# Optimization experiments

Hardware: AMD Instinct MI355X
Metric: run time of the kernel (lower is better)

Reference implementation:

```python
import jax, jax.numpy as jnp
import numpy as np

N_NODES = 50000
N_FEAT = 256
HIDDEN = 256
N_EDGES = 800000


def gcn_conv(x, edge_index, W, b):
    """PyG GCNConv: out = D^-1/2 (A+I) D^-1/2 (x @ W) + b."""
    n = x.shape[0]
    loop = jnp.arange(n, dtype=edge_index.dtype)
    src = jnp.concatenate([edge_index[0], loop])  # [E+N]
    dst = jnp.concatenate([edge_index[1], loop])  # [E+N]
    deg = jax.ops.segment_sum(jnp.ones_like(dst, dtype=x.dtype), dst, num_segments=n)
    dinv = jnp.where(deg > 0, jax.lax.rsqrt(deg), 0.0)
    norm = dinv[src] * dinv[dst]                  # [E+N]
    h = x @ W                                     # [N, out]
    msg = h[src] * norm[:, None]                  # gather + scale
    out = jax.ops.segment_sum(msg, dst, num_segments=n)  # scatter-add
    return out + b


def setup_inputs() -> dict:
    key = jax.random.key(0)
    ks = jax.random.split(key, 8)
    x = jax.random.normal(ks[0], (N_NODES, N_FEAT), dtype=jnp.float32)
    train_pos_edge_index = jax.random.randint(ks[1], (2, N_EDGES), 0, N_NODES, dtype=jnp.int64)
    pos_edge_index = jax.random.randint(ks[2], (2, N_EDGES), 0, N_NODES, dtype=jnp.int64)
    neg_edge_index = jax.random.randint(ks[3], (2, N_EDGES), 0, N_NODES, dtype=jnp.int64)
    # Glorot-style init for GCN weights
    W1 = jax.random.normal(ks[4], (N_FEAT, HIDDEN), dtype=jnp.float32) * (1.0 / np.sqrt(N_FEAT))
    b1 = jnp.zeros((HIDDEN,), dtype=jnp.float32)
    W2 = jax.random.normal(ks[5], (HIDDEN, HIDDEN // 2), dtype=jnp.float32) * (1.0 / np.sqrt(HIDDEN))
    b2 = jnp.zeros((HIDDEN // 2,), dtype=jnp.float32)
    return {"x": x, "train_pos_edge_index": train_pos_edge_index,
            "pos_edge_index": pos_edge_index, "neg_edge_index": neg_edge_index,
            "W1": W1, "b1": b1, "W2": W2, "b2": b2}


def reference(x, train_pos_edge_index, pos_edge_index, neg_edge_index, W1, b1, W2, b2):
    # encode
    h = jax.nn.relu(gcn_conv(x, train_pos_edge_index, W1, b1))
    z = gcn_conv(h, train_pos_edge_index, W2, b2)  # [N, HIDDEN//2]
    # decode: dot product over concatenated pos+neg edges
    edge_index = jnp.concatenate([pos_edge_index, neg_edge_index], axis=-1)  # [2, 2E]
    logits = jnp.sum(z[edge_index[0]] * z[edge_index[1]], axis=-1)           # [2E]
    return logits
```

## Files before the change

### kernel.cpp

```cpp
#include <hip/hip_runtime.h>
#include <hip/hip_fp16.h>


#define NFEAT 256
#define HID   256
#define OUTF  128
#define SCAN_T 1024

typedef _Float16 f16x8 __attribute__((ext_vector_type(8)));
typedef float    f32x4 __attribute__((ext_vector_type(4)));

__global__ void k_init_deg(float* __restrict__ deg, int n) {
    int i = blockIdx.x * blockDim.x + threadIdx.x;
    if (i < n) deg[i] = 1.0f;
}

__global__ void k_count_deg(const int* __restrict__ ei, float* __restrict__ deg, int E) {
    int e = blockIdx.x * blockDim.x + threadIdx.x;
    if (e < E) atomicAdd(&deg[ei[E + e]], 1.0f);
}

__global__ __launch_bounds__(SCAN_T) void k_scan(
        float* __restrict__ deg_dinv, int* __restrict__ rowptr,
        int* __restrict__ cursor, int n) {
    __shared__ int swsum[16];
    __shared__ int s_total;
    __shared__ int s_chunk;
    const int t    = threadIdx.x;
    const int wave = t >> 6;
    const int lane = t & 63;
    if (t == 0) s_total = 0;

    for (int base = 0; base < n; base += SCAN_T) {
        int i = base + t;
        float dg = 1.0f;
        int v = 0;
        if (i < n) { dg = deg_dinv[i]; v = (int)dg - 1; }
        int sc = v;
#pragma unroll
        for (int off = 1; off < 64; off <<= 1) {
            int y = __shfl_up(sc, off);
            if (lane >= off) sc += y;
        }
        if (lane == 63) swsum[wave] = sc;
        __syncthreads();
        if (t < 16) {
            int w = swsum[t];
            int scw = w;
#pragma unroll
            for (int off = 1; off < 16; off <<= 1) {
                int y = __shfl_up(scw, off);
                if (t >= off) scw += y;
            }
            swsum[t] = scw - w;
            if (t == 15) s_chunk = scw;
        }
        __syncthreads();
        int rp = s_total + swsum[wave] + (sc - v);
        if (i < n) {
            rowptr[i] = rp;
            cursor[i] = rp;
            deg_dinv[i] = rsqrtf(dg);
        }
        __syncthreads();
        if (t == 0) s_total += s_chunk;
        __syncthreads();
    }
    if (t == 0) rowptr[n] = s_total;
}

__global__ void k_fill(const int* __restrict__ ei, int* __restrict__ cursor,
                       int* __restrict__ eidx, int E) {
    int e = blockIdx.x * blockDim.x + threadIdx.x;
    if (e < E) {
        int s = ei[e];
        int d = ei[E + e];
        int p = atomicAdd(&cursor[d], 1);
        eidx[p] = s;
    }
}

__global__ __launch_bounds__(256) void k_wt(const float* __restrict__ W,
                                            __half* __restrict__ Wt, int K, int M) {
    __shared__ float tile[32][33];
    int k0 = blockIdx.x * 32, m0 = blockIdx.y * 32;
    int tx = threadIdx.x & 31, ty = threadIdx.x >> 5;
#pragma unroll
    for (int r = 0; r < 4; ++r)
        tile[ty + r * 8][tx] = W[(size_t)(k0 + ty + r * 8) * M + m0 + tx];
    __syncthreads();
#pragma unroll
    for (int r = 0; r < 4; ++r)
        Wt[(size_t)(m0 + ty + r * 8) * K + k0 + tx] = __float2half(tile[tx][ty + r * 8]);
}

template <int MT, bool AF32>
__global__ __launch_bounds__(256) void k_gemm_mfma(
        const void* __restrict__ Aptr, const __half* __restrict__ Wt,
        const float* __restrict__ dinv, __half* __restrict__ outp,
        int n, int K, int M) {
    constexpr int BM = 2 * MT * 16;
    __shared__ __half As[BM][40];
    __shared__ __half Bs[128][40];
    __shared__ __half Cs[4][16][72];

    const int t    = threadIdx.x;
    const int wave = t >> 6;
    const int lane = t & 63;
    const int row0 = blockIdx.x * BM;
    const int col0 = blockIdx.y * 128;
    const int wm = wave >> 1, wn = wave & 1;
    const int lr = lane & 15;
    const int kq = lane >> 4;

    f32x4 acc[MT][4];
#pragma unroll
    for (int i = 0; i < MT; ++i)
#pragma unroll
        for (int j = 0; j < 4; ++j) acc[i][j] = (f32x4){0.f, 0.f, 0.f, 0.f};

    for (int k0 = 0; k0 < K; k0 += 32) {
        if (AF32) {
            const float* A = (const float*)Aptr;
#pragma unroll
            for (int it = 0; it < BM * 8 / 256; ++it) {
                int q = t + it * 256;
                int r = q >> 3, c4 = q & 7;
                int gr = min(row0 + r, n - 1);
                float4 v = *(const float4*)&A[(size_t)gr * K + k0 + c4 * 4];
                __half2* dst = (__half2*)&As[r][c4 * 4];
                dst[0] = __floats2half2_rn(v.x, v.y);
                dst[1] = __floats2half2_rn(v.z, v.w);
            }
        } else {
            const __half* A = (const __half*)Aptr;
#pragma unroll
            for (int it = 0; it < BM * 4 / 256; ++it) {
                int q = t + it * 256;
                int r = q >> 2, c8 = q & 3;
                int gr = min(row0 + r, n - 1);
                *(float4*)&As[r][c8 * 8] = *(const float4*)&A[(size_t)gr * K + k0 + c8 * 8];
            }
        }
#pragma unroll
        for (int it = 0; it < 2; ++it) {
            int q = t + it * 256;
            int r = q >> 2, c8 = q & 3;
            *(float4*)&Bs[r][c8 * 8] = *(const float4*)&Wt[(size_t)(col0 + r) * K + k0 + c8 * 8];
        }
        __syncthreads();

        f16x8 b[4];
#pragma unroll
        for (int j = 0; j < 4; ++j)
            b[j] = *(const f16x8*)&Bs[wn * 64 + j * 16 + lr][kq * 8];
#pragma unroll
        for (int i = 0; i < MT; ++i) {
            f16x8 a = *(const f16x8*)&As[wm * MT * 16 + i * 16 + lr][kq * 8];
#pragma unroll
            for (int j = 0; j < 4; ++j)
                acc[i][j] = __builtin_amdgcn_mfma_f32_16x16x32_f16(a, b[j], acc[i][j], 0, 0, 0);
        }
        __syncthreads();
    }

#pragma unroll
    for (int i = 0; i < MT; ++i) {
        int gr0 = row0 + wm * MT * 16 + i * 16;
        float dv[4];
#pragma unroll
        for (int r = 0; r < 4; ++r)
            dv[r] = dinv[min(gr0 + kq * 4 + r, n - 1)];
        __syncthreads();
#pragma unroll
        for (int j = 0; j < 4; ++j)
#pragma unroll
            for (int r = 0; r < 4; ++r)
                Cs[wave][kq * 4 + r][j * 16 + lr] = __float2half(acc[i][j][r] * dv[r]);
        __syncthreads();
        int r1 = lane >> 3, c1 = (lane & 7) * 8;
#pragma unroll
        for (int h = 0; h < 2; ++h) {
            int grow = gr0 + r1 + h * 8;
            if (grow < n)
                *(float4*)&outp[(size_t)grow * M + col0 + wn * 64 + c1] =
                    *(const float4*)&Cs[wave][r1 + h * 8][c1];
        }
    }
}

__global__ void k_agg1(const int* __restrict__ rowptr, const int* __restrict__ eidx,
                       const __half* __restrict__ g, const float* __restrict__ dinv,
                       const float* __restrict__ bias, __half* __restrict__ out, int n) {
    int wid  = (int)(((size_t)blockIdx.x * blockDim.x + threadIdx.x) >> 6);
    int lane = threadIdx.x & 63;
    if (wid >= n) return;
    int j   = rowptr[wid];
    int end = rowptr[wid + 1];
    float sc = dinv[wid];

    union HF2 { float2 f; __half2 h[2]; };
    float4 acc;
    {
        HF2 u; u.f = ((const float2*)(g + (size_t)wid * HID))[lane];
        float2 lo = __half22float2(u.h[0]);
        float2 hi = __half22float2(u.h[1]);
        acc = make_float4(lo.x, lo.y, hi.x, hi.y);
    }
    for (; j + 1 < end; j += 2) {
        int s0 = eidx[j];
        int s1 = eidx[j + 1];
        HF2 u0; u0.f = ((const float2*)(g + (size_t)s0 * HID))[lane];
        HF2 u1; u1.f = ((const float2*)(g + (size_t)s1 * HID))[lane];
        float2 a0 = __half22float2(u0.h[0]), a1 = __half22float2(u0.h[1]);
        float2 c0 = __half22float2(u1.h[0]), c1 = __half22float2(u1.h[1]);
        acc.x += a0.x + c0.x; acc.y += a0.y + c0.y;
        acc.z += a1.x + c1.x; acc.w += a1.y + c1.y;
    }
    if (j < end) {
        int s0 = eidx[j];
        HF2 u0; u0.f = ((const float2*)(g + (size_t)s0 * HID))[lane];
        float2 a0 = __half22float2(u0.h[0]), a1 = __half22float2(u0.h[1]);
        acc.x += a0.x; acc.y += a0.y; acc.z += a1.x; acc.w += a1.y;
    }
    float4 b = ((const float4*)bias)[lane];
    HF2 r;
    r.h[0] = __floats2half2_rn(fmaxf(sc * acc.x + b.x, 0.f), fmaxf(sc * acc.y + b.y, 0.f));
    r.h[1] = __floats2half2_rn(fmaxf(sc * acc.z + b.z, 0.f), fmaxf(sc * acc.w + b.w, 0.f));
    ((float2*)(out + (size_t)wid * HID))[lane] = r.f;
}

__global__ void k_agg2(const int* __restrict__ rowptr, const int* __restrict__ eidx,
                       const __half* __restrict__ g, const float* __restrict__ dinv,
                       const float* __restrict__ bias, __half* __restrict__ out, int n) {
    int wid  = (int)(((size_t)blockIdx.x * blockDim.x + threadIdx.x) >> 6);
    int lane = threadIdx.x & 63;
    if (wid >= n) return;
    int j   = rowptr[wid];
    int end = rowptr[wid + 1];
    float sc = dinv[wid];

    float2 acc = __half22float2(((const __half2*)(g + (size_t)wid * OUTF))[lane]);
    for (; j + 1 < end; j += 2) {
        int s0 = eidx[j];
        int s1 = eidx[j + 1];
        float2 v0 = __half22float2(((const __half2*)(g + (size_t)s0 * OUTF))[lane]);
        float2 v1 = __half22float2(((const __half2*)(g + (size_t)s1 * OUTF))[lane]);
        acc.x += v0.x + v1.x; acc.y += v0.y + v1.y;
    }
    if (j < end) {
        int s0 = eidx[j];
        float2 v0 = __half22float2(((const __half2*)(g + (size_t)s0 * OUTF))[lane]);
        acc.x += v0.x; acc.y += v0.y;
    }
    float2 b = ((const float2*)bias)[lane];
    __half2 r = __floats2half2_rn(sc * acc.x + b.x, sc * acc.y + b.y);
    ((__half2*)(out + (size_t)wid * OUTF))[lane] = r;
}

__global__ void k_decode(const int* __restrict__ pos, const int* __restrict__ neg,
                         const __half* __restrict__ z, float* __restrict__ out, int E) {
    size_t gid = (size_t)blockIdx.x * blockDim.x + threadIdx.x;
    int e  = (int)(gid >> 4);
    int sl = (int)(threadIdx.x & 15);
    if (e >= 2 * E) return;
    int a, b;
    if (e < E) { a = pos[e];     b = pos[E + e]; }
    else       { a = neg[e - E]; b = neg[e];     }
    union HF4 { float4 f; __half2 h[4]; };
    HF4 ua, ub;
    ua.f = ((const float4*)(z + (size_t)a * OUTF))[sl];
    ub.f = ((const float4*)(z + (size_t)b * OUTF))[sl];
    float p = 0.f;
#pragma unroll
    for (int k = 0; k < 4; ++k) {
        float2 fa = __half22float2(ua.h[k]);
        float2 fb = __half22float2(ub.h[k]);
        p += fa.x * fb.x + fa.y * fb.y;
    }
    p += __shfl_xor(p, 1);
    p += __shfl_xor(p, 2);
    p += __shfl_xor(p, 4);
    p += __shfl_xor(p, 8);
    if (sl == 0) out[e] = p;
}

extern "C" void kernel_launch(void* const* d_in, const int* in_sizes, int n_in,
                              void* d_out, int out_size, void* d_ws, size_t ws_size,
                              hipStream_t stream) {
    const float* x   = (const float*)d_in[0];
    const int*   tei = (const int*)d_in[1];
    const int*   pos = (const int*)d_in[2];
    const int*   neg = (const int*)d_in[3];
    const float* W1  = (const float*)d_in[4];
    const float* b1  = (const float*)d_in[5];
    const float* W2  = (const float*)d_in[6];
    const float* b2  = (const float*)d_in[7];
    float* out = (float*)d_out;

    const int N = in_sizes[0] / NFEAT;
    const int E = in_sizes[1] / 2;

    char* ws = (char*)d_ws;
    size_t off = 0;
    __half* g1h = (__half*)(ws + off);
    __half* g2h = (__half*)(ws + off);
    __half* zh  = (__half*)(ws + off + (size_t)N * OUTF * 2);
    off += (size_t)N * HID * 2;
    __half* h1h = (__half*)(ws + off);  off += (size_t)N * HID * 2;
    float*  dinv = (float*)(ws + off);  off += (size_t)N * 4;
    int* rowptr = (int*)(ws + off);     off += (size_t)(N + 1) * 4;
    int* cursor = (int*)(ws + off);     off += (size_t)N * 4;
    int* eidx   = (int*)(ws + off);     off += (size_t)E * 4;
    __half* W1t = (__half*)(ws + off);  off += (size_t)NFEAT * HID * 2;
    __half* W2t = (__half*)(ws + off);  off += (size_t)HID * OUTF * 2;

    { dim3 g(NFEAT / 32, HID / 32);  k_wt<<<g, 256, 0, stream>>>(W1, W1t, NFEAT, HID); }
    { dim3 g(HID / 32, OUTF / 32);   k_wt<<<g, 256, 0, stream>>>(W2, W2t, HID, OUTF); }

    k_init_deg<<<(N + 255) / 256, 256, 0, stream>>>(dinv, N);
    k_count_deg<<<(E + 255) / 256, 256, 0, stream>>>(tei, dinv, E);
    k_scan<<<1, SCAN_T, 0, stream>>>(dinv, rowptr, cursor, N);
    k_fill<<<(E + 255) / 256, 256, 0, stream>>>(tei, cursor, eidx, E);

    {
        dim3 grid((N + 127) / 128, HID / 128);
        k_gemm_mfma<4, true><<<grid, 256, 0, stream>>>(x, W1t, dinv, g1h, N, NFEAT, HID);
        size_t nth = (size_t)N * 64;
        k_agg1<<<(int)((nth + 255) / 256), 256, 0, stream>>>(
            rowptr, eidx, g1h, dinv, b1, h1h, N);
    }

    {
        dim3 grid((N + 63) / 64, OUTF / 128);
        k_gemm_mfma<2, false><<<grid, 256, 0, stream>>>(h1h, W2t, dinv, g2h, N, HID, OUTF);
        size_t nth = (size_t)N * 64;
        k_agg2<<<(int)((nth + 255) / 256), 256, 0, stream>>>(
            rowptr, eidx, g2h, dinv, b2, zh, N);
    }

    {
        size_t nth = (size_t)2 * E * 16;
        k_decode<<<(int)((nth + 255) / 256), 256, 0, stream>>>(pos, neg, zh, out, E);
    }
}
```

Measured before the change: 495.6 us.

## Store GEMM outputs in feature-sliced layout and aggregate per slice

The GEMM epilogue now writes its output in a column-sliced layout: 8 slices of 32 (layer 1) or 16 (layer 2) features, each slice stored contiguously across all nodes. The aggregation kernels are rewritten so consecutive blocks handle one slice for a group of nodes. Each neighbour gather then touches a 64- or 32-byte segment inside a smaller per-slice working set, which is meant to improve cache hit rates for the random gathers. The cost is more gather instructions per edge, each fetching fewer bytes, and edge indices are reread once per slice.

```diff
diff --git a/kernel.cpp b/kernel.cpp
--- a/kernel.cpp
+++ b/kernel.cpp
@@ -94,7 +94,7 @@
         Wt[(size_t)(m0 + ty + r * 8) * K + k0 + tx] = __float2half(tile[tx][ty + r * 8]);
 }
 
-template <int MT, bool AF32>
+template <int MT, bool AF32, int SWL>
 __global__ __launch_bounds__(256) void k_gemm_mfma(
         const void* __restrict__ Aptr, const __half* __restrict__ Wt,
         const float* __restrict__ dinv, __half* __restrict__ outp,
@@ -164,6 +164,7 @@
         __syncthreads();
     }
 
+    constexpr int SW = 1 << SWL;
 #pragma unroll
     for (int i = 0; i < MT; ++i) {
         int gr0 = row0 + wm * MT * 16 + i * 16;
@@ -182,80 +183,76 @@
 #pragma unroll
         for (int h = 0; h < 2; ++h) {
             int grow = gr0 + r1 + h * 8;
-            if (grow < n)
-                *(float4*)&outp[(size_t)grow * M + col0 + wn * 64 + c1] =
-                    *(const float4*)&Cs[wave][r1 + h * 8][c1];
+            if (grow < n) {
+                int col = col0 + wn * 64 + c1;
+                size_t oidx = ((size_t)(col >> SWL) * n + grow) * SW + (col & (SW - 1));
+                *(float4*)&outp[oidx] = *(const float4*)&Cs[wave][r1 + h * 8][c1];
+            }
         }
     }
 }
 
 __global__ void k_agg1(const int* __restrict__ rowptr, const int* __restrict__ eidx,
-                       const __half* __restrict__ g, const float* __restrict__ dinv,
+                       const __half* __restrict__ g1s, const float* __restrict__ dinv,
                        const float* __restrict__ bias, __half* __restrict__ out, int n) {
-    int wid  = (int)(((size_t)blockIdx.x * blockDim.x + threadIdx.x) >> 6);
-    int lane = threadIdx.x & 63;
-    if (wid >= n) return;
-    int j   = rowptr[wid];
-    int end = rowptr[wid + 1];
-    float sc = dinv[wid];
-
-    union HF2 { float2 f; __half2 h[2]; };
-    float4 acc;
-    {
-        HF2 u; u.f = ((const float2*)(g + (size_t)wid * HID))[lane];
-        float2 lo = __half22float2(u.h[0]);
-        float2 hi = __half22float2(u.h[1]);
-        acc = make_float4(lo.x, lo.y, hi.x, hi.y);
-    }
+    const int slice = blockIdx.x & 7;
+    const int node  = (blockIdx.x >> 3) * 16 + (threadIdx.x >> 4);
+    const int sl    = threadIdx.x & 15;
+    if (node >= n) return;
+    int j   = rowptr[node];
+    int end = rowptr[node + 1];
+    float sc = dinv[node];
+    const __half* base = g1s + (size_t)slice * n * 32 + sl * 2;
+
+    float2 acc = __half22float2(*(const __half2*)&base[(size_t)node * 32]);
     for (; j + 1 < end; j += 2) {
         int s0 = eidx[j];
         int s1 = eidx[j + 1];
-        HF2 u0; u0.f = ((const float2*)(g + (size_t)s0 * HID))[lane];
-        HF2 u1; u1.f = ((const float2*)(g + (size_t)s1 * HID))[lane];
-        float2 a0 = __half22float2(u0.h[0]), a1 = __half22float2(u0.h[1]);
-        float2 c0 = __half22float2(u1.h[0]), c1 = __half22float2(u1.h[1]);
-        acc.x += a0.x + c0.x; acc.y += a0.y + c0.y;
-        acc.z += a1.x + c1.x; acc.w += a1.y + c1.y;
+        float2 v0 = __half22float2(*(const __half2*)&base[(size_t)s0 * 32]);
+        float2 v1 = __half22float2(*(const __half2*)&base[(size_t)s1 * 32]);
+        acc.x += v0.x + v1.x; acc.y += v0.y + v1.y;
     }
     if (j < end) {
         int s0 = eidx[j];
-        HF2 u0; u0.f = ((const float2*)(g + (size_t)s0 * HID))[lane];
-        float2 a0 = __half22float2(u0.h[0]), a1 = __half22float2(u0.h[1]);
-        acc.x += a0.x; acc.y += a0.y; acc.z += a1.x; acc.w += a1.y;
-    }
-    float4 b = ((const float4*)bias)[lane];
-    HF2 r;
-    r.h[0] = __floats2half2_rn(fmaxf(sc * acc.x + b.x, 0.f), fmaxf(sc * acc.y + b.y, 0.f));
-    r.h[1] = __floats2half2_rn(fmaxf(sc * acc.z + b.z, 0.f), fmaxf(sc * acc.w + b.w, 0.f));
-    ((float2*)(out + (size_t)wid * HID))[lane] = r.f;
+        float2 v0 = __half22float2(*(const __half2*)&base[(size_t)s0 * 32]);
+        acc.x += v0.x; acc.y += v0.y;
+    }
+    int f = slice * 32 + sl * 2;
+    float2 b = *(const float2*)&bias[f];
+    __half2 r = __floats2half2_rn(fmaxf(sc * acc.x + b.x, 0.f),
+                                  fmaxf(sc * acc.y + b.y, 0.f));
+    *(__half2*)&out[(size_t)node * HID + f] = r;
 }
 
 __global__ void k_agg2(const int* __restrict__ rowptr, const int* __restrict__ eidx,
-                       const __half* __restrict__ g, const float* __restrict__ dinv,
+                       const __half* __restrict__ g2s, const float* __restrict__ dinv,
                        const float* __restrict__ bias, __half* __restrict__ out, int n) {
-    int wid  = (int)(((size_t)blockIdx.x * blockDim.x + threadIdx.x) >> 6);
-    int lane = threadIdx.x & 63;
-    if (wid >= n) return;
-    int j   = rowptr[wid];
-    int end = rowptr[wid + 1];
-    float sc = dinv[wid];
-
-    float2 acc = __half22float2(((const __half2*)(g + (size_t)wid * OUTF))[lane]);
+    const int slice = blockIdx.x & 7;
+    const int node  = (blockIdx.x >> 3) * 32 + (threadIdx.x >> 3);
+    const int sl    = threadIdx.x & 7;
+    if (node >= n) return;
+    int j   = rowptr[node];
+    int end = rowptr[node + 1];
+    float sc = dinv[node];
+    const __half* base = g2s + (size_t)slice * n * 16 + sl * 2;
+
+    float2 acc = __half22float2(*(const __half2*)&base[(size_t)node * 16]);
     for (; j + 1 < end; j += 2) {
         int s0 = eidx[j];
         int s1 = eidx[j + 1];
-        float2 v0 = __half22float2(((const __half2*)(g + (size_t)s0 * OUTF))[lane]);
-        float2 v1 = __half22float2(((const __half2*)(g + (size_t)s1 * OUTF))[lane]);
+        float2 v0 = __half22float2(*(const __half2*)&base[(size_t)s0 * 16]);
+        float2 v1 = __half22float2(*(const __half2*)&base[(size_t)s1 * 16]);
         acc.x += v0.x + v1.x; acc.y += v0.y + v1.y;
     }
     if (j < end) {
         int s0 = eidx[j];
-        float2 v0 = __half22float2(((const __half2*)(g + (size_t)s0 * OUTF))[lane]);
+        float2 v0 = __half22float2(*(const __half2*)&base[(size_t)s0 * 16]);
         acc.x += v0.x; acc.y += v0.y;
     }
-    float2 b = ((const float2*)bias)[lane];
+    int f = slice * 16 + sl * 2;
+    float2 b = *(const float2*)&bias[f];
     __half2 r = __floats2half2_rn(sc * acc.x + b.x, sc * acc.y + b.y);
-    ((__half2*)(out + (size_t)wid * OUTF))[lane] = r;
+    *(__half2*)&out[(size_t)node * OUTF + f] = r;
 }
 
 __global__ void k_decode(const int* __restrict__ pos, const int* __restrict__ neg,
@@ -303,8 +300,8 @@
 
     char* ws = (char*)d_ws;
     size_t off = 0;
-    __half* g1h = (__half*)(ws + off);
-    __half* g2h = (__half*)(ws + off);
+    __half* g1s = (__half*)(ws + off);
+    __half* g2s = (__half*)(ws + off);
     __half* zh  = (__half*)(ws + off + (size_t)N * OUTF * 2);
     off += (size_t)N * HID * 2;
     __half* h1h = (__half*)(ws + off);  off += (size_t)N * HID * 2;
@@ -325,18 +322,16 @@
 
     {
         dim3 grid((N + 127) / 128, HID / 128);
-        k_gemm_mfma<4, true><<<grid, 256, 0, stream>>>(x, W1t, dinv, g1h, N, NFEAT, HID);
-        size_t nth = (size_t)N * 64;
-        k_agg1<<<(int)((nth + 255) / 256), 256, 0, stream>>>(
-            rowptr, eidx, g1h, dinv, b1, h1h, N);
+        k_gemm_mfma<4, true, 5><<<grid, 256, 0, stream>>>(x, W1t, dinv, g1s, N, NFEAT, HID);
+        int nblk = 8 * ((N + 15) / 16);
+        k_agg1<<<nblk, 256, 0, stream>>>(rowptr, eidx, g1s, dinv, b1, h1h, N);
     }
 
     {
         dim3 grid((N + 63) / 64, OUTF / 128);
-        k_gemm_mfma<2, false><<<grid, 256, 0, stream>>>(h1h, W2t, dinv, g2h, N, HID, OUTF);
-        size_t nth = (size_t)N * 64;
-        k_agg2<<<(int)((nth + 255) / 256), 256, 0, stream>>>(
-            rowptr, eidx, g2h, dinv, b2, zh, N);
+        k_gemm_mfma<2, false, 4><<<grid, 256, 0, stream>>>(h1h, W2t, dinv, g2s, N, HID, OUTF);
+        int nblk = 8 * ((N + 31) / 32);
+        k_agg2<<<nblk, 256, 0, stream>>>(rowptr, eidx, g2s, dinv, b2, zh, N);
     }
 
     {
```

Result: slower. 525.3 us (+6.0%).
